# Kernel optimization log

Measured on AMD Instinct MI355X. Metric: run time of the kernel, lower is better.

The kernel has to match this reference:

```python
import jax, jax.numpy as jnp
import numpy as np

N_NODES = 100000   # n_entities + n_users
N_REL = 16
N_EDGES = 1600000
D = 64             # entity_dim == relation_dim
DIMS = [64, 32, 16, 16, 8]
NEG_SLOPE = 0.01   # nn.LeakyReLU default
EPS = 1e-12        # F.normalize default eps


def setup_inputs() -> dict:
    key = jax.random.key(0)
    ks = jax.random.split(key, 16)
    def lin(k, i, o):
        return jax.random.normal(k, (i, o), jnp.float32) / np.sqrt(i)
    inp = {
        'emb': jax.random.normal(ks[0], (N_NODES, D), jnp.float32) * 0.1,
        'rel_embed': jax.random.normal(ks[1], (N_REL, D), jnp.float32) * 0.1,
        'W_R': jax.random.normal(ks[2], (N_REL, D, D), jnp.float32) / np.sqrt(D),
        'W0': lin(ks[3], DIMS[0], DIMS[1]), 'b0': jnp.zeros((DIMS[1],), jnp.float32),
        'W1': lin(ks[4], DIMS[1], DIMS[2]), 'b1': jnp.zeros((DIMS[2],), jnp.float32),
        'W2': lin(ks[5], DIMS[2], DIMS[3]), 'b2': jnp.zeros((DIMS[3],), jnp.float32),
        'W3': lin(ks[6], DIMS[3], DIMS[4]), 'b3': jnp.zeros((DIMS[4],), jnp.float32),
        'src': jax.random.randint(ks[7], (N_EDGES,), 0, N_NODES, jnp.int32),
        'dst': jnp.sort(jax.random.randint(ks[8], (N_EDGES,), 0, N_NODES, jnp.int32)),
        'etype': jax.random.randint(ks[9], (N_EDGES,), 0, N_REL, jnp.int32),
    }
    return inp


def _lrelu(x):
    return jnp.where(x >= 0, x, NEG_SLOPE * x)


def _l2norm(x):
    n = jnp.sqrt(jnp.sum(x * x, axis=1, keepdims=True))
    return x / jnp.maximum(n, EPS)


def reference(emb, rel_embed, W_R, W0, b0, W1, b1, W2, b2, W3, b3, src, dst, etype):
    N = emb.shape[0]
    # --- compute_attention: TransR-style per-edge score (vectorized over relations) ---
    # all_mul[n, r, :] = emb[n] @ W_R[r]  (equivalent to the per-relation loop)
    all_mul = jnp.einsum('nd,rdk->nrk', emb, W_R)          # (N, R, D)
    r_mul_t = all_mul[src, etype]                          # edges.src transformed (E, D)
    r_mul_h = all_mul[dst, etype]                          # edges.dst transformed (E, D)
    att = jnp.sum(r_mul_t * jnp.tanh(r_mul_h + rel_embed[etype]), axis=-1)  # (E,)
    # --- edge softmax grouped by destination node ---
    m = jax.ops.segment_max(att, dst, num_segments=N)
    e = jnp.exp(att - m[dst])
    s = jax.ops.segment_sum(e, dst, num_segments=N)
    att = (e / s[dst])[:, None]                            # (E, 1)

    Ws = [(W0, b0), (W1, b1), (W2, b2), (W3, b3)]
    results = []
    for index in range(1, 5):
        ego = emb
        all_embed = [ego]
        for i, (W, b) in enumerate(Ws):
            if i < index:
                # u_mul_e('node','att') + sum over incoming edges
                N_h = jax.ops.segment_sum(att * ego[src], dst, num_segments=N)
                ego = _lrelu((ego + N_h) @ W + b)          # gcn aggregator, type 0
            else:
                ego = _lrelu(ego @ W + b)                  # type 1: linear only
            all_embed.append(_l2norm(ego))
        results.append(jnp.concatenate(all_embed, axis=1))  # (N, 136)
    return jnp.stack(results)                               # (4, N, 136)
```

## Files before the change

### kernel.cpp

```cpp
#include <hip/hip_runtime.h>
#include <hip/hip_bf16.h>
#include <math.h>

#define N_NODES 100000
#define N_RELS 16
#define N_EDGES 1600000
#define OUTW 136
#define NEG_SLOPE 0.01f
#define RES ((size_t)N_NODES * OUTW)

typedef __attribute__((ext_vector_type(8))) short short8;
typedef __attribute__((ext_vector_type(8))) unsigned short ushort8;
typedef __attribute__((ext_vector_type(4))) float f32x4;

__device__ __forceinline__ float lrelu(float x) { return x >= 0.f ? x : NEG_SLOPE * x; }
__device__ __forceinline__ float fast_rcp(float x) { return __builtin_amdgcn_rcpf(x); }
__device__ __forceinline__ float fast_tanh(float x) {
    float e = __expf(2.f * x);
    return 1.f - 2.f * fast_rcp(e + 1.f);
}
__device__ __forceinline__ float bf1(unsigned short u) { union { unsigned u; float f; } v; v.u = ((unsigned)u) << 16; return v.f; }
__device__ __forceinline__ unsigned short f2bf(float f) {
    union { float f; unsigned u; } v; v.f = f;
    unsigned x = v.u + 0x7FFF + ((v.u >> 16) & 1);
    return (unsigned short)(x >> 16);
}

__global__ __launch_bounds__(256) void k_prep(const float* __restrict__ emb, unsigned short* __restrict__ embB,
                                              const float* __restrict__ WR, unsigned short* __restrict__ WT,
                                              const float* __restrict__ W0, const float* __restrict__ W1,
                                              const float* __restrict__ W2, const float* __restrict__ W3,
                                              float* __restrict__ WLT,
                                              const int* __restrict__ dst, int* __restrict__ offs,
                                              int* __restrict__ cnt) {
    int blk = blockIdx.x, tid = threadIdx.x;
    if (blk < 6250) {
        int id = blk * 256 + tid;
        float4 v = *(const float4*)(emb + (size_t)id * 4);
        ushort4 o; o.x = f2bf(v.x); o.y = f2bf(v.y); o.z = f2bf(v.z); o.w = f2bf(v.w);
        *(ushort4*)(embB + (size_t)id * 4) = o;
    } else if (blk < 6506) {
        int id = (blk - 6250) * 256 + tid;
        int r = id >> 12, rem = id & 4095, n = rem >> 6, k = rem & 63;
        WT[id] = f2bf(WR[(r << 12) + (k << 6) + n]);
    } else if (blk < 6518) {
        int id = (blk - 6506) * 256 + tid;
        if (id < 2944) {
            float v;
            if (id < 2048)      { int c = id >> 6, k = id & 63;                  v = W0[k * 32 + c]; }
            else if (id < 2560) { int r = id - 2048; int c = r >> 5, k = r & 31; v = W1[k * 16 + c]; }
            else if (id < 2816) { int r = id - 2560; int c = r >> 4, k = r & 15; v = W2[k * 16 + c]; }
            else                { int r = id - 2816; int c = r >> 4, k = r & 15; v = W3[k * 8 + c]; }
            WLT[id] = v;
        }
    } else if (blk < 6909) {
        int n = (blk - 6518) * 256 + tid;
        if (n <= N_NODES) {
            int lo = 0, hi = N_EDGES;
            while (lo < hi) { int mid = (lo + hi) >> 1; if (dst[mid] < n) lo = mid + 1; else hi = mid; }
            offs[n] = lo;
        }
    } else {
        if (tid < 16) cnt[tid] = 0;
    }
}

__global__ __launch_bounds__(256) void k_hist(const int* __restrict__ etype, int* __restrict__ cnt) {
    __shared__ int lcnt[16];
    int tid = threadIdx.x;
    if (tid < 16) lcnt[tid] = 0;
    __syncthreads();
    atomicAdd(&lcnt[etype[blockIdx.x * 256 + tid]], 1);
    __syncthreads();
    if (tid < 16 && lcnt[tid]) atomicAdd(&cnt[tid], lcnt[tid]);
}

__global__ void k_scan(const int* __restrict__ cnt, int* __restrict__ roff, int* __restrict__ cur) {
    if (threadIdx.x == 0) {
        int a = 0;
        for (int r = 0; r < 16; ++r) { roff[r] = a; cur[r] = a; a += cnt[r]; }
        roff[16] = a;
    }
}

__global__ __launch_bounds__(256) void k_scatter(const int* __restrict__ etype,
                                                 const int* __restrict__ src,
                                                 const int* __restrict__ dst,
                                                 int* __restrict__ cur, int* __restrict__ eperm,
                                                 int* __restrict__ srcp, int* __restrict__ dstp) {
    __shared__ int lcnt[16], lbase[16], loff[16];
    int tid = threadIdx.x;
    if (tid < 16) { lcnt[tid] = 0; loff[tid] = 0; }
    __syncthreads();
    int e = blockIdx.x * 256 + tid;
    int t = etype[e];
    atomicAdd(&lcnt[t], 1);
    __syncthreads();
    if (tid < 16) lbase[tid] = lcnt[tid] ? atomicAdd(&cur[tid], lcnt[tid]) : 0;
    __syncthreads();
    int rank = atomicAdd(&loff[t], 1);
    int pos = lbase[t] + rank;
    eperm[pos] = e;
    srcp[pos] = src[e];
    dstp[pos] = dst[e];
}

__global__ __launch_bounds__(256) void k_gemm_mfma(const unsigned short* __restrict__ embB,
                                                   const unsigned short* __restrict__ WT,
                                                   unsigned short* __restrict__ bufs, int nrel) {
    int tid = threadIdx.x, w = tid >> 6, l = tid & 63;
    int row0 = blockIdx.x * 128 + w * 32;
    int rlo = l & 15, rhi = l >> 4;

    short8 a[2][2];
    #pragma unroll
    for (int rb = 0; rb < 2; ++rb)
        #pragma unroll
        for (int ks = 0; ks < 2; ++ks) {
            int r = row0 + rb * 16 + rlo;
            if (r >= N_NODES) r = N_NODES - 1;
            a[rb][ks] = *(const short8*)(embB + (size_t)r * 64 + ks * 32 + rhi * 8);
        }

    for (int cr = 0; cr < nrel; ++cr) {
        const unsigned short* wt = WT + ((size_t)cr << 12);
        f32x4 acc[2][4];
        #pragma unroll
        for (int rb = 0; rb < 2; ++rb)
            #pragma unroll
            for (int cb = 0; cb < 4; ++cb) acc[rb][cb] = (f32x4){0.f, 0.f, 0.f, 0.f};
        #pragma unroll
        for (int cb = 0; cb < 4; ++cb) {
            short8 b0 = *(const short8*)(wt + (cb * 16 + rlo) * 64 + rhi * 8);
            short8 b1 = *(const short8*)(wt + (cb * 16 + rlo) * 64 + 32 + rhi * 8);
            acc[0][cb] = __builtin_amdgcn_mfma_f32_16x16x32_bf16(a[0][0], b0, acc[0][cb], 0, 0, 0);
            acc[0][cb] = __builtin_amdgcn_mfma_f32_16x16x32_bf16(a[0][1], b1, acc[0][cb], 0, 0, 0);
            acc[1][cb] = __builtin_amdgcn_mfma_f32_16x16x32_bf16(a[1][0], b0, acc[1][cb], 0, 0, 0);
            acc[1][cb] = __builtin_amdgcn_mfma_f32_16x16x32_bf16(a[1][1], b1, acc[1][cb], 0, 0, 0);
        }
        unsigned short* ob = bufs + (size_t)cr * N_NODES * 64;
        #pragma unroll
        for (int rb = 0; rb < 2; ++rb)
            #pragma unroll
            for (int cb = 0; cb < 4; ++cb)
                #pragma unroll
                for (int i = 0; i < 4; ++i) {
                    int gr = row0 + rb * 16 + rhi * 4 + i;
                    if (gr < N_NODES) ob[(size_t)gr * 64 + cb * 16 + rlo] = f2bf(acc[rb][cb][i]);
                }
    }
}

__global__ __launch_bounds__(256) void k_edge_att4(const unsigned short* __restrict__ bufs,
                                                   const float* __restrict__ rel,
                                                   const int* __restrict__ srcp,
                                                   const int* __restrict__ dstp,
                                                   const int* __restrict__ eperm,
                                                   const int* __restrict__ roff,
                                                   int c0, int nc, float* __restrict__ att) {
    int lo = roff[c0];
    int cnt = roff[c0 + nc] - lo;
    int bnd0 = (nc > 1) ? roff[c0 + 1] - lo : 0x7fffffff;
    int bnd1 = (nc > 2) ? roff[c0 + 2] - lo : 0x7fffffff;
    int bnd2 = (nc > 3) ? roff[c0 + 3] - lo : 0x7fffffff;
    int tid = threadIdx.x, lane = tid & 63;
    int sub = lane >> 3, lj = lane & 7, d0 = lj * 8;
    int gw = (blockIdx.x * 256 + tid) >> 6;
    int nw = (gridDim.x * 256) >> 6;
    for (int i = gw * 8 + sub; i < cnt; i += nw * 8) {
        int t = (i >= bnd0) + (i >= bnd1) + (i >= bnd2);
        const unsigned short* bb = bufs + (size_t)t * N_NODES * 64;
        const float* rr = rel + (size_t)(c0 + t) * 64 + d0;
        size_t s = (size_t)srcp[lo + i], dn = (size_t)dstp[lo + i];
        ushort8 tv = *(const ushort8*)(bb + s * 64 + d0);
        ushort8 hv = *(const ushort8*)(bb + dn * 64 + d0);
        float4 r0 = *(const float4*)(rr);
        float4 r1 = *(const float4*)(rr + 4);
        float v = bf1(tv[0]) * fast_tanh(bf1(hv[0]) + r0.x)
                + bf1(tv[1]) * fast_tanh(bf1(hv[1]) + r0.y)
                + bf1(tv[2]) * fast_tanh(bf1(hv[2]) + r0.z)
                + bf1(tv[3]) * fast_tanh(bf1(hv[3]) + r0.w)
                + bf1(tv[4]) * fast_tanh(bf1(hv[4]) + r1.x)
                + bf1(tv[5]) * fast_tanh(bf1(hv[5]) + r1.y)
                + bf1(tv[6]) * fast_tanh(bf1(hv[6]) + r1.z)
                + bf1(tv[7]) * fast_tanh(bf1(hv[7]) + r1.w);
        #pragma unroll
        for (int m = 1; m < 8; m <<= 1) v += __shfl_xor(v, m);
        if (lj == 0) att[eperm[lo + i]] = v;
    }
}

__global__ __launch_bounds__(256) void k_softmax(float* __restrict__ att, const int* __restrict__ offs) {
    int tid = threadIdx.x;
    int n = blockIdx.x * 32 + (tid >> 3);
    int j = tid & 7;
    int b = offs[n], e = offs[n + 1];
    if (b >= e) return;
    float m = -INFINITY;
    for (int i = b + j; i < e; i += 8) m = fmaxf(m, att[i]);
    #pragma unroll
    for (int s = 4; s >= 1; s >>= 1) m = fmaxf(m, __shfl_xor(m, s));
    float sum = 0.f;
    for (int i = b + j; i < e; i += 8) { float v = __expf(att[i] - m); att[i] = v; sum += v; }
    #pragma unroll
    for (int s = 4; s >= 1; s >>= 1) sum += __shfl_xor(sum, s);
    float inv = fast_rcp(sum);
    for (int i = b + j; i < e; i += 8) att[i] *= inv;
}

__global__ __launch_bounds__(256) void k_dense0(const float* __restrict__ emb,
                                                const float* __restrict__ WLT,
                                                float* __restrict__ Y0,
                                                float* __restrict__ out) {
    int tid = threadIdx.x, w = tid >> 6, l = tid & 63;
    int c = l & 31, g = l >> 5;
    float Wreg[32];
    #pragma unroll
    for (int kk = 0; kk < 32; ++kk) Wreg[kk] = WLT[(size_t)c * 64 + g * 32 + kk];
    int nw = gridDim.x * 4;
    for (int n = blockIdx.x * 4 + w; n < N_NODES; n += nw) {
        const float* xr = emb + (size_t)n * 64;
        float v = xr[l];
        #pragma unroll
        for (int r = 0; r < 4; ++r)
            out[(size_t)r * RES + (size_t)n * OUTW + l] = v;
        float o = 0.f;
        #pragma unroll
        for (int kk = 0; kk < 32; kk += 4) {
            float4 xv = *(const float4*)(xr + g * 32 + kk);
            o += xv.x * Wreg[kk] + xv.y * Wreg[kk + 1] + xv.z * Wreg[kk + 2] + xv.w * Wreg[kk + 3];
        }
        o += __shfl_xor(o, 32);
        if (l < 32) Y0[(size_t)n * 32 + c] = o;
    }
}

template<int D, int DN, int COL, int RSTART, bool PROJ>
__global__ __launch_bounds__(256) void k_aggF(const float* __restrict__ Y,
                                              const float* __restrict__ att,
                                              const int* __restrict__ src,
                                              const int* __restrict__ offs,
                                              const float* __restrict__ bias,
                                              const float* __restrict__ WTn,
                                              float* __restrict__ Yn,
                                              float* __restrict__ out) {
    constexpr int E = D / 4;
    constexpr int S = 64 / E;
    constexpr int G = PROJ ? (64 / DN) : 1;
    constexpr int KS = PROJ ? (D / G) : 1;
    __shared__ float xm[4][PROJ ? D : 4];
    int tid = threadIdx.x, w = tid >> 6, l = tid & 63;
    int n = blockIdx.x * 4 + w;
    int b = offs[n], e = offs[n + 1];
    int je = l & (E - 1), slot = l / E;

    float Wreg[KS];
    if constexpr (PROJ) {
        int c = l & (DN - 1), g = l / DN;
        #pragma unroll
        for (int kk = 0; kk < KS; ++kk) Wreg[kk] = WTn[(size_t)c * D + g * KS + kk];
    }

    float4 a = make_float4(0.f, 0.f, 0.f, 0.f);
    int i = b + slot;
    for (; i + S < e; i += 2 * S) {
        float t0 = att[i], t1 = att[i + S];
        float4 p0 = *(const float4*)(Y + (size_t)src[i]     * D + 4 * je);
        float4 p1 = *(const float4*)(Y + (size_t)src[i + S] * D + 4 * je);
        a.x += t0 * p0.x + t1 * p1.x;
        a.y += t0 * p0.y + t1 * p1.y;
        a.z += t0 * p0.z + t1 * p1.z;
        a.w += t0 * p0.w + t1 * p1.w;
    }
    for (; i < e; i += S) {
        float t0 = att[i];
        float4 p0 = *(const float4*)(Y + (size_t)src[i] * D + 4 * je);
        a.x += t0 * p0.x; a.y += t0 * p0.y; a.z += t0 * p0.z; a.w += t0 * p0.w;
    }
    #pragma unroll
    for (int st = E; st < 64; st <<= 1) {
        a.x += __shfl_xor(a.x, st); a.y += __shfl_xor(a.y, st);
        a.z += __shfl_xor(a.z, st); a.w += __shfl_xor(a.w, st);
    }
    float4 q  = *(const float4*)(Y + (size_t)n * D + 4 * je);
    float4 bi = *(const float4*)(bias + 4 * je);
    float4 u;
    u.x = lrelu(a.x + q.x + bi.x);
    u.y = lrelu(a.y + q.y + bi.y);
    u.z = lrelu(a.z + q.z + bi.z);
    u.w = lrelu(a.w + q.w + bi.w);
    float ss = u.x * u.x + u.y * u.y + u.z * u.z + u.w * u.w;
    #pragma unroll
    for (int st = 1; st < E; st <<= 1) ss += __shfl_xor(ss, st);
    float inv = fast_rcp(fmaxf(sqrtf(ss), 1e-12f));
    if (slot < 4 - RSTART) {
        float4 nr = make_float4(u.x * inv, u.y * inv, u.z * inv, u.w * inv);
        *(float4*)(out + (size_t)(RSTART + slot) * RES + (size_t)n * OUTW + COL + 4 * je) = nr;
    }
    if constexpr (PROJ) {
        if (slot == S - 1) *(float4*)&xm[w][4 * je] = u;
        __builtin_amdgcn_s_waitcnt(0);
        __builtin_amdgcn_sched_barrier(0);
        int c = l & (DN - 1), g = l / DN;
        float o = 0.f;
        if constexpr (KS >= 4) {
            #pragma unroll
            for (int kk = 0; kk < KS; kk += 4) {
                float4 xv = *(const float4*)&xm[w][g * KS + kk];
                o += xv.x * Wreg[kk] + xv.y * Wreg[kk + 1] + xv.z * Wreg[kk + 2] + xv.w * Wreg[kk + 3];
            }
        } else {
            float2 xv = *(const float2*)&xm[w][g * KS];
            o += xv.x * Wreg[0] + xv.y * Wreg[1];
        }
        #pragma unroll
        for (int st = DN; st < 64; st <<= 1) o += __shfl_xor(o, st);
        if (l < DN) Yn[(size_t)n * DN + c] = o;
    }
}

__global__ __launch_bounds__(256) void k_bchain(const float* __restrict__ Y1,
                                                const float* __restrict__ Y2,
                                                const float* __restrict__ Y3,
                                                const float* __restrict__ WLT,
                                                const float* __restrict__ b1,
                                                const float* __restrict__ b2,
                                                const float* __restrict__ b3,
                                                float* __restrict__ out) {
    __shared__ float W2s[16][17], W3s[8][17];
    __shared__ float bb1[16], bb2[16], bb3[8];
    __shared__ float mid[16][17], mid2[16][17];
    int tid = threadIdx.x;
    if (tid < 256) W2s[tid >> 4][tid & 15] = WLT[2560 + tid];
    if (tid < 128) W3s[tid >> 4][tid & 15] = WLT[2816 + tid];
    if (tid < 16) bb1[tid] = b1[tid];
    if (tid >= 32 && tid < 48) bb2[tid - 32] = b2[tid - 32];
    if (tid >= 64 && tid < 72) bb3[tid - 64] = b3[tid - 64];
    __syncthreads();

    int grp = tid >> 4, lj = tid & 15;
    int seg = blockIdx.x / 6250;
    int nb = blockIdx.x % 6250;
    int n = nb * 16 + grp;

    if (seg == 0) {
        float u1 = lrelu(Y1[(size_t)n * 16 + lj] + bb1[lj]);
        mid[grp][lj] = u1;
        float ss = u1 * u1;
        #pragma unroll
        for (int m = 8; m >= 1; m >>= 1) ss += __shfl_xor(ss, m);
        out[(size_t)n * OUTW + 96 + lj] = u1 * fast_rcp(fmaxf(sqrtf(ss), 1e-12f));
        __builtin_amdgcn_s_waitcnt(0);
        __builtin_amdgcn_sched_barrier(0);
        float o2 = bb2[lj];
        #pragma unroll
        for (int k = 0; k < 16; ++k) o2 += mid[grp][k] * W2s[lj][k];
        float u2 = lrelu(o2);
        mid2[grp][lj] = u2;
        float s2 = u2 * u2;
        #pragma unroll
        for (int m = 8; m >= 1; m >>= 1) s2 += __shfl_xor(s2, m);
        out[(size_t)n * OUTW + 112 + lj] = u2 * fast_rcp(fmaxf(sqrtf(s2), 1e-12f));
        __builtin_amdgcn_s_waitcnt(0);
        __builtin_amdgcn_sched_barrier(0);
        if (lj < 8) {
            float o3 = bb3[lj];
            #pragma unroll
            for (int k = 0; k < 16; ++k) o3 += mid2[grp][k] * W3s[lj][k];
            float u3 = lrelu(o3);
            float s3 = u3 * u3;
            #pragma unroll
            for (int m = 4; m >= 1; m >>= 1) s3 += __shfl_xor(s3, m);
            out[(size_t)n * OUTW + 128 + lj] = u3 * fast_rcp(fmaxf(sqrtf(s3), 1e-12f));
        }
    } else if (seg == 1) {
        float u2 = lrelu(Y2[(size_t)n * 16 + lj] + bb2[lj]);
        mid[grp][lj] = u2;
        float s2 = u2 * u2;
        #pragma unroll
        for (int m = 8; m >= 1; m >>= 1) s2 += __shfl_xor(s2, m);
        out[RES + (size_t)n * OUTW + 112 + lj] = u2 * fast_rcp(fmaxf(sqrtf(s2), 1e-12f));
        __builtin_amdgcn_s_waitcnt(0);
        __builtin_amdgcn_sched_barrier(0);
        if (lj < 8) {
            float o3 = bb3[lj];
            #pragma unroll
            for (int k = 0; k < 16; ++k) o3 += mid[grp][k] * W3s[lj][k];
            float u3 = lrelu(o3);
            float s3 = u3 * u3;
            #pragma unroll
            for (int m = 4; m >= 1; m >>= 1) s3 += __shfl_xor(s3, m);
            out[RES + (size_t)n * OUTW + 128 + lj] = u3 * fast_rcp(fmaxf(sqrtf(s3), 1e-12f));
        }
    } else {
        if (lj < 8) {
            float u3 = lrelu(Y3[(size_t)n * 8 + lj] + bb3[lj]);
            float s3 = u3 * u3;
            #pragma unroll
            for (int m = 4; m >= 1; m >>= 1) s3 += __shfl_xor(s3, m);
            out[2 * RES + (size_t)n * OUTW + 128 + lj] = u3 * fast_rcp(fmaxf(sqrtf(s3), 1e-12f));
        }
    }
}

extern "C" void kernel_launch(void* const* d_in, const int* in_sizes, int n_in,
                              void* d_out, int out_size, void* d_ws, size_t ws_size,
                              hipStream_t stream) {
    (void)in_sizes; (void)n_in; (void)out_size;
    const float* emb = (const float*)d_in[0];
    const float* rel_embed = (const float*)d_in[1];
    const float* W_R = (const float*)d_in[2];
    const float* W0 = (const float*)d_in[3];  const float* b0 = (const float*)d_in[4];
    const float* W1 = (const float*)d_in[5];  const float* b1 = (const float*)d_in[6];
    const float* W2 = (const float*)d_in[7];  const float* b2 = (const float*)d_in[8];
    const float* W3 = (const float*)d_in[9];  const float* b3 = (const float*)d_in[10];
    const int* src = (const int*)d_in[11];
    const int* dst = (const int*)d_in[12];
    const int* etype = (const int*)d_in[13];
    float* out = (float*)d_out;

    char* p = (char*)d_ws;
    auto alloc = [&](size_t bytes) { char* q = p; p += (bytes + 255) & ~(size_t)255; return q; };
    int* offs  = (int*)alloc((size_t)(N_NODES + 1) * 4);
    float* att = (float*)alloc((size_t)N_EDGES * 4);
    int* eperm = (int*)alloc((size_t)N_EDGES * 4);
    int* srcp  = (int*)alloc((size_t)N_EDGES * 4);
    int* dstp  = (int*)alloc((size_t)N_EDGES * 4);
    int* cnt   = (int*)alloc(64);
    int* roff  = (int*)alloc(68);
    int* cur   = (int*)alloc(64);
    unsigned short* embB = (unsigned short*)alloc((size_t)N_NODES * 64 * 2);
    unsigned short* WT   = (unsigned short*)alloc((size_t)65536 * 2);
    float* WLT = (float*)alloc((size_t)2944 * 4);
    float* Y0  = (float*)alloc((size_t)N_NODES * 32 * 4);
    float* Y1  = (float*)alloc((size_t)N_NODES * 16 * 4);
    float* Y2  = (float*)alloc((size_t)N_NODES * 16 * 4);
    float* Y3  = (float*)alloc((size_t)N_NODES * 8 * 4);
    size_t fixed = (size_t)(p - (char*)d_ws);
    size_t per_rel = (size_t)N_NODES * 64 * 2;
    int chunk = 1;
    if (ws_size > fixed + per_rel)
        chunk = (int)((ws_size - fixed) / per_rel);
    if (chunk > 4) chunk = 4;
    if (chunk < 1) chunk = 1;
    unsigned short* allbuf = (unsigned short*)p;

    k_prep<<<6910, 256, 0, stream>>>(emb, embB, W_R, WT, W0, W1, W2, W3, WLT, dst, offs, cnt);
    k_hist<<<N_EDGES / 256, 256, 0, stream>>>(etype, cnt);
    k_scan<<<1, 64, 0, stream>>>(cnt, roff, cur);
    k_scatter<<<N_EDGES / 256, 256, 0, stream>>>(etype, src, dst, cur, eperm, srcp, dstp);

    for (int c0 = 0; c0 < N_RELS; c0 += chunk) {
        int nc = N_RELS - c0 < chunk ? N_RELS - c0 : chunk;
        k_gemm_mfma<<<(N_NODES + 127) / 128, 256, 0, stream>>>(embB, WT + (size_t)c0 * 4096, allbuf, nc);
        k_edge_att4<<<2048, 256, 0, stream>>>(allbuf, rel_embed, srcp, dstp, eperm, roff, c0, nc, att);
    }
    k_softmax<<<N_NODES / 32, 256, 0, stream>>>(att, offs);

    k_dense0<<<3125, 256, 0, stream>>>(emb, WLT, Y0, out);

    k_aggF<32, 16,  64, 0, true ><<<N_NODES / 4, 256, 0, stream>>>(Y0, att, src, offs, b0, WLT + 2048, Y1, out);
    k_aggF<16, 16,  96, 1, true ><<<N_NODES / 4, 256, 0, stream>>>(Y1, att, src, offs, b1, WLT + 2560, Y2, out);
    k_aggF<16,  8, 112, 2, true ><<<N_NODES / 4, 256, 0, stream>>>(Y2, att, src, offs, b2, WLT + 2816, Y3, out);
    k_aggF< 8,  8, 128, 3, false><<<N_NODES / 4, 256, 0, stream>>>(Y3, att, src, offs, b3, nullptr, nullptr, out);

    k_bchain<<<18750, 256, 0, stream>>>(Y1, Y2, Y3, WLT, b1, b2, b3, out);
}
```

Measured before the change: 628.3 us.

## Fuse per-relation projection into edge attention, computing transforms per edge via MFMA

Removes the materialised per-relation node projection buffers (N x 64 bf16 per relation, written in chunks) and instead computes the src and dst projections on the fly for each edge. Edges, already grouped by relation, are processed in 16-edge MFMA tiles that use that relation's weights. A new block-offset table is produced in the scan kernel to map tiles to relations. This trades roughly 3.2M row-projections of recompute, against 1.6M from the precomputed buffers, for the removal of about 200MB of intermediate traffic and several kernel launches.

```diff
diff --git a/kernel.cpp b/kernel.cpp
--- a/kernel.cpp
+++ b/kernel.cpp
@@ -10,7 +10,6 @@
 #define RES ((size_t)N_NODES * OUTW)
 
 typedef __attribute__((ext_vector_type(8))) short short8;
-typedef __attribute__((ext_vector_type(8))) unsigned short ushort8;
 typedef __attribute__((ext_vector_type(4))) float f32x4;
 
 __device__ __forceinline__ float lrelu(float x) { return x >= 0.f ? x : NEG_SLOPE * x; }
@@ -19,7 +18,6 @@
     float e = __expf(2.f * x);
     return 1.f - 2.f * fast_rcp(e + 1.f);
 }
-__device__ __forceinline__ float bf1(unsigned short u) { union { unsigned u; float f; } v; v.u = ((unsigned)u) << 16; return v.f; }
 __device__ __forceinline__ unsigned short f2bf(float f) {
     union { float f; unsigned u; } v; v.f = f;
     unsigned x = v.u + 0x7FFF + ((v.u >> 16) & 1);
@@ -75,11 +73,15 @@
     if (tid < 16 && lcnt[tid]) atomicAdd(&cnt[tid], lcnt[tid]);
 }
 
-__global__ void k_scan(const int* __restrict__ cnt, int* __restrict__ roff, int* __restrict__ cur) {
+__global__ void k_scan(const int* __restrict__ cnt, int* __restrict__ roff, int* __restrict__ cur,
+                       int* __restrict__ bo) {
     if (threadIdx.x == 0) {
-        int a = 0;
-        for (int r = 0; r < 16; ++r) { roff[r] = a; cur[r] = a; a += cnt[r]; }
-        roff[16] = a;
+        int a = 0, nb = 0;
+        for (int r = 0; r < 16; ++r) {
+            roff[r] = a; cur[r] = a; bo[r] = nb;
+            a += cnt[r]; nb += (cnt[r] + 15) >> 4;
+        }
+        roff[16] = a; bo[16] = nb;
     }
 }
 
@@ -105,88 +107,84 @@
     dstp[pos] = dst[e];
 }
 
-__global__ __launch_bounds__(256) void k_gemm_mfma(const unsigned short* __restrict__ embB,
+__global__ __launch_bounds__(256) void k_edge_attF(const unsigned short* __restrict__ embB,
                                                    const unsigned short* __restrict__ WT,
-                                                   unsigned short* __restrict__ bufs, int nrel) {
-    int tid = threadIdx.x, w = tid >> 6, l = tid & 63;
-    int row0 = blockIdx.x * 128 + w * 32;
-    int rlo = l & 15, rhi = l >> 4;
-
-    short8 a[2][2];
-    #pragma unroll
-    for (int rb = 0; rb < 2; ++rb)
-        #pragma unroll
-        for (int ks = 0; ks < 2; ++ks) {
-            int r = row0 + rb * 16 + rlo;
-            if (r >= N_NODES) r = N_NODES - 1;
-            a[rb][ks] = *(const short8*)(embB + (size_t)r * 64 + ks * 32 + rhi * 8);
-        }
-
-    for (int cr = 0; cr < nrel; ++cr) {
-        const unsigned short* wt = WT + ((size_t)cr << 12);
-        f32x4 acc[2][4];
-        #pragma unroll
-        for (int rb = 0; rb < 2; ++rb)
-            #pragma unroll
-            for (int cb = 0; cb < 4; ++cb) acc[rb][cb] = (f32x4){0.f, 0.f, 0.f, 0.f};
-        #pragma unroll
-        for (int cb = 0; cb < 4; ++cb) {
-            short8 b0 = *(const short8*)(wt + (cb * 16 + rlo) * 64 + rhi * 8);
-            short8 b1 = *(const short8*)(wt + (cb * 16 + rlo) * 64 + 32 + rhi * 8);
-            acc[0][cb] = __builtin_amdgcn_mfma_f32_16x16x32_bf16(a[0][0], b0, acc[0][cb], 0, 0, 0);
-            acc[0][cb] = __builtin_amdgcn_mfma_f32_16x16x32_bf16(a[0][1], b1, acc[0][cb], 0, 0, 0);
-            acc[1][cb] = __builtin_amdgcn_mfma_f32_16x16x32_bf16(a[1][0], b0, acc[1][cb], 0, 0, 0);
-            acc[1][cb] = __builtin_amdgcn_mfma_f32_16x16x32_bf16(a[1][1], b1, acc[1][cb], 0, 0, 0);
-        }
-        unsigned short* ob = bufs + (size_t)cr * N_NODES * 64;
-        #pragma unroll
-        for (int rb = 0; rb < 2; ++rb)
-            #pragma unroll
-            for (int cb = 0; cb < 4; ++cb)
-                #pragma unroll
-                for (int i = 0; i < 4; ++i) {
-                    int gr = row0 + rb * 16 + rhi * 4 + i;
-                    if (gr < N_NODES) ob[(size_t)gr * 64 + cb * 16 + rlo] = f2bf(acc[rb][cb][i]);
-                }
-    }
-}
-
-__global__ __launch_bounds__(256) void k_edge_att4(const unsigned short* __restrict__ bufs,
                                                    const float* __restrict__ rel,
                                                    const int* __restrict__ srcp,
                                                    const int* __restrict__ dstp,
                                                    const int* __restrict__ eperm,
                                                    const int* __restrict__ roff,
-                                                   int c0, int nc, float* __restrict__ att) {
-    int lo = roff[c0];
-    int cnt = roff[c0 + nc] - lo;
-    int bnd0 = (nc > 1) ? roff[c0 + 1] - lo : 0x7fffffff;
-    int bnd1 = (nc > 2) ? roff[c0 + 2] - lo : 0x7fffffff;
-    int bnd2 = (nc > 3) ? roff[c0 + 3] - lo : 0x7fffffff;
-    int tid = threadIdx.x, lane = tid & 63;
-    int sub = lane >> 3, lj = lane & 7, d0 = lj * 8;
-    int gw = (blockIdx.x * 256 + tid) >> 6;
-    int nw = (gridDim.x * 256) >> 6;
-    for (int i = gw * 8 + sub; i < cnt; i += nw * 8) {
-        int t = (i >= bnd0) + (i >= bnd1) + (i >= bnd2);
-        const unsigned short* bb = bufs + (size_t)t * N_NODES * 64;
-        const float* rr = rel + (size_t)(c0 + t) * 64 + d0;
-        size_t s = (size_t)srcp[lo + i], dn = (size_t)dstp[lo + i];
-        ushort8 tv = *(const ushort8*)(bb + s * 64 + d0);
-        ushort8 hv = *(const ushort8*)(bb + dn * 64 + d0);
-        float4 r0 = *(const float4*)(rr);
-        float4 r1 = *(const float4*)(rr + 4);
-        float v = bf1(tv[0]) * fast_tanh(bf1(hv[0]) + r0.x)
-                + bf1(tv[1]) * fast_tanh(bf1(hv[1]) + r0.y)
-                + bf1(tv[2]) * fast_tanh(bf1(hv[2]) + r0.z)
-                + bf1(tv[3]) * fast_tanh(bf1(hv[3]) + r0.w)
-                + bf1(tv[4]) * fast_tanh(bf1(hv[4]) + r1.x)
-                + bf1(tv[5]) * fast_tanh(bf1(hv[5]) + r1.y)
-                + bf1(tv[6]) * fast_tanh(bf1(hv[6]) + r1.z)
-                + bf1(tv[7]) * fast_tanh(bf1(hv[7]) + r1.w);
-        #pragma unroll
-        for (int m = 1; m < 8; m <<= 1) v += __shfl_xor(v, m);
-        if (lj == 0) att[eperm[lo + i]] = v;
+                                                   const int* __restrict__ bo,
+                                                   float* __restrict__ att) {
+    __shared__ int sro[17], sbo[17];
+    int tid = threadIdx.x;
+    if (tid < 17) { sro[tid] = roff[tid]; sbo[tid] = bo[tid]; }
+    __syncthreads();
+    int w = tid >> 6, l = tid & 63;
+    int rlo = l & 15, rhi = l >> 4;
+    int gw = blockIdx.x * 4 + w;
+    int nw = gridDim.x * 4;
+    int NB = sbo[16];
+    int per = (NB + nw - 1) / nw;
+    int start = gw * per;
+    int end = start + per < NB ? start + per : NB;
+    if (start >= end) return;
+
+    int r = 0;
+    while (sbo[r + 1] <= start) ++r;
+
+    short8 bfr[4][2];
+    float relv[4];
+    {
+        const unsigned short* wt = WT + ((size_t)r << 12);
+        #pragma unroll
+        for (int cb = 0; cb < 4; ++cb) {
+            bfr[cb][0] = *(const short8*)(wt + (cb * 16 + rlo) * 64 + rhi * 8);
+            bfr[cb][1] = *(const short8*)(wt + (cb * 16 + rlo) * 64 + 32 + rhi * 8);
+            relv[cb] = rel[r * 64 + cb * 16 + rlo];
+        }
+    }
+
+    for (int g = start; g < end; ++g) {
+        if (g >= sbo[r + 1]) {
+            while (sbo[r + 1] <= g) ++r;
+            const unsigned short* wt = WT + ((size_t)r << 12);
+            #pragma unroll
+            for (int cb = 0; cb < 4; ++cb) {
+                bfr[cb][0] = *(const short8*)(wt + (cb * 16 + rlo) * 64 + rhi * 8);
+                bfr[cb][1] = *(const short8*)(wt + (cb * 16 + rlo) * 64 + 32 + rhi * 8);
+                relv[cb] = rel[r * 64 + cb * 16 + rlo];
+            }
+        }
+        int i0 = sro[r] + (g - sbo[r]) * 16;
+        int hi = sro[r + 1];
+        int ea = i0 + rlo; if (ea >= hi) ea = hi - 1;
+        size_t sA = (size_t)srcp[ea], sB = (size_t)dstp[ea];
+        short8 at0 = *(const short8*)(embB + sA * 64 + rhi * 8);
+        short8 at1 = *(const short8*)(embB + sA * 64 + 32 + rhi * 8);
+        short8 ah0 = *(const short8*)(embB + sB * 64 + rhi * 8);
+        short8 ah1 = *(const short8*)(embB + sB * 64 + 32 + rhi * 8);
+        f32x4 accT[4], accH[4];
+        #pragma unroll
+        for (int cb = 0; cb < 4; ++cb) {
+            accT[cb] = (f32x4){0.f, 0.f, 0.f, 0.f};
+            accH[cb] = (f32x4){0.f, 0.f, 0.f, 0.f};
+            accT[cb] = __builtin_amdgcn_mfma_f32_16x16x32_bf16(at0, bfr[cb][0], accT[cb], 0, 0, 0);
+            accT[cb] = __builtin_amdgcn_mfma_f32_16x16x32_bf16(at1, bfr[cb][1], accT[cb], 0, 0, 0);
+            accH[cb] = __builtin_amdgcn_mfma_f32_16x16x32_bf16(ah0, bfr[cb][0], accH[cb], 0, 0, 0);
+            accH[cb] = __builtin_amdgcn_mfma_f32_16x16x32_bf16(ah1, bfr[cb][1], accH[cb], 0, 0, 0);
+        }
+        #pragma unroll
+        for (int i = 0; i < 4; ++i) {
+            float s = 0.f;
+            #pragma unroll
+            for (int cb = 0; cb < 4; ++cb)
+                s += accT[cb][i] * fast_tanh(accH[cb][i] + relv[cb]);
+            s += __shfl_xor(s, 1); s += __shfl_xor(s, 2);
+            s += __shfl_xor(s, 4); s += __shfl_xor(s, 8);
+            int idx = i0 + rhi * 4 + i;
+            if (rlo == 0 && idx < hi) att[eperm[idx]] = s;
+        }
     }
 }
 
@@ -406,7 +404,7 @@
 extern "C" void kernel_launch(void* const* d_in, const int* in_sizes, int n_in,
                               void* d_out, int out_size, void* d_ws, size_t ws_size,
                               hipStream_t stream) {
-    (void)in_sizes; (void)n_in; (void)out_size;
+    (void)in_sizes; (void)n_in; (void)out_size; (void)ws_size;
     const float* emb = (const float*)d_in[0];
     const float* rel_embed = (const float*)d_in[1];
     const float* W_R = (const float*)d_in[2];
@@ -429,6 +427,7 @@
     int* cnt   = (int*)alloc(64);
     int* roff  = (int*)alloc(68);
     int* cur   = (int*)alloc(64);
+    int* bo    = (int*)alloc(68);
     unsigned short* embB = (unsigned short*)alloc((size_t)N_NODES * 64 * 2);
     unsigned short* WT   = (unsigned short*)alloc((size_t)65536 * 2);
     float* WLT = (float*)alloc((size_t)2944 * 4);
@@ -436,25 +435,13 @@
     float* Y1  = (float*)alloc((size_t)N_NODES * 16 * 4);
     float* Y2  = (float*)alloc((size_t)N_NODES * 16 * 4);
     float* Y3  = (float*)alloc((size_t)N_NODES * 8 * 4);
-    size_t fixed = (size_t)(p - (char*)d_ws);
-    size_t per_rel = (size_t)N_NODES * 64 * 2;
-    int chunk = 1;
-    if (ws_size > fixed + per_rel)
-        chunk = (int)((ws_size - fixed) / per_rel);
-    if (chunk > 4) chunk = 4;
-    if (chunk < 1) chunk = 1;
-    unsigned short* allbuf = (unsigned short*)p;
 
     k_prep<<<6910, 256, 0, stream>>>(emb, embB, W_R, WT, W0, W1, W2, W3, WLT, dst, offs, cnt);
     k_hist<<<N_EDGES / 256, 256, 0, stream>>>(etype, cnt);
-    k_scan<<<1, 64, 0, stream>>>(cnt, roff, cur);
+    k_scan<<<1, 64, 0, stream>>>(cnt, roff, cur, bo);
     k_scatter<<<N_EDGES / 256, 256, 0, stream>>>(etype, src, dst, cur, eperm, srcp, dstp);
 
-    for (int c0 = 0; c0 < N_RELS; c0 += chunk) {
-        int nc = N_RELS - c0 < chunk ? N_RELS - c0 : chunk;
-        k_gemm_mfma<<<(N_NODES + 127) / 128, 256, 0, stream>>>(embB, WT + (size_t)c0 * 4096, allbuf, nc);
-        k_edge_att4<<<2048, 256, 0, stream>>>(allbuf, rel_embed, srcp, dstp, eperm, roff, c0, nc, att);
-    }
+    k_edge_attF<<<2048, 256, 0, stream>>>(embB, WT, rel_embed, srcp, dstp, eperm, roff, bo, att);
     k_softmax<<<N_NODES / 32, 256, 0, stream>>>(att, offs);
 
     k_dense0<<<3125, 256, 0, stream>>>(emb, WLT, Y0, out);
```

New measurement: 554.5 us. -11.7%, faster.
